# Kernel tuning notes

Measured on AMD Instinct MI355X. Metric: run time of the kernel, lower is better.

Reference implementation:

```python
import jax, jax.numpy as jnp
import numpy as np

B, T, CIN = 64, 1024, 1
H1, H2 = 128, 256  # hidden sizes hardcoded in the flax module


def setup_inputs() -> dict:
    key = jax.random.key(0)
    ks = jax.random.split(key, 24)
    n = lambda k, shp: jax.random.normal(k, shp, dtype=jnp.float32) * 0.05
    z = lambda shp: jnp.zeros(shp, jnp.float32)
    return {
        "X": n(ks[0], (B, T, CIN)),
        "conv_w": n(ks[1], (4, CIN, 16)), "conv_b": z((16,)),
        # gate layout: [i, f, g, o] concatenated, as in flax LSTMCell
        "Wi1": n(ks[2], (16, 4 * H1)), "Wh1": n(ks[3], (H1, 4 * H1)), "b1": z((4 * H1,)),
        "Wi2": n(ks[4], (16, 4 * H1)), "Wh2": n(ks[5], (H1, 4 * H1)), "b2": z((4 * H1,)),
        "Wi3": n(ks[6], (2 * H1, 4 * H2)), "Wh3": n(ks[7], (H2, 4 * H2)), "b3": z((4 * H2,)),
        "Wi4": n(ks[8], (2 * H1, 4 * H2)), "Wh4": n(ks[9], (H2, 4 * H2)), "b4": z((4 * H2,)),
        "attW": n(ks[10], (2 * H2, 128)), "attWb": z((128,)),
        "attV": n(ks[11], (128, 1)), "attVb": z((1,)),
        "d1W": n(ks[12], (2 * H2, 128)), "d1b": z((128,)),
        "d2W": n(ks[13], (128, 1)), "d2b": z((1,)),
    }


def _lstm(x, Wi, Wh, b, hidden):
    """Forward-in-time LSTM over x:(B,T,D) -> outputs (B,T,hidden). flax gate order i,f,g,o."""
    Bb = x.shape[0]

    def step(carry, xt):
        c, h = carry
        z = xt @ Wi + h @ Wh + b  # (B, 4H)
        i, f, g, o = jnp.split(z, 4, axis=-1)
        c = jax.nn.sigmoid(f) * c + jax.nn.sigmoid(i) * jnp.tanh(g)
        h = jax.nn.sigmoid(o) * jnp.tanh(c)
        return (c, h), h

    init = (jnp.zeros((Bb, hidden), x.dtype), jnp.zeros((Bb, hidden), x.dtype))
    _, hs = jax.lax.scan(step, init, jnp.swapaxes(x, 0, 1))  # (T,B,H)
    return jnp.swapaxes(hs, 0, 1)


def reference(X, conv_w, conv_b, Wi1, Wh1, b1, Wi2, Wh2, b2, Wi3, Wh3, b3,
              Wi4, Wh4, b4, attW, attWb, attV, attVb, d1W, d1b, d2W, d2b):
    # Conv1d, SAME padding (flax default)
    x = jax.lax.conv_general_dilated(X, conv_w, (1,), 'SAME',
                                     dimension_numbers=('NWC', 'WIO', 'NWC')) + conv_b
    # NOTE: original flips the FEATURE axis (axis=-1), not time — reproduced faithfully
    x1 = _lstm(x, Wi1, Wh1, b1, H1)
    x2 = _lstm(jnp.flip(x, axis=-1), Wi2, Wh2, b2, H1)
    x = jnp.concatenate([x1, x2], axis=-1)  # (B,T,256)
    x3 = _lstm(x, Wi3, Wh3, b3, H2)
    x4 = _lstm(jnp.flip(x, axis=-1), Wi4, Wh4, b4, H2)
    enc = jnp.concatenate([x3, x4], axis=-1)  # (B,T,512)
    # attention pooling over time
    score = jnp.tanh(enc @ attW + attWb) @ attV + attVb  # (B,T,1)
    w = jax.nn.softmax(score, axis=1)
    ctx = jnp.sum(w * enc, axis=1)  # (B,512)
    h = jnp.tanh(ctx @ d1W + d1b)  # dropout deterministic -> identity
    return h @ d2W + d2b  # (B,1)
```

## Files before the change

### kernel.cpp

```cpp
#include <hip/hip_runtime.h>
#include <hip/hip_fp16.h>

#define B_   64
#define T_   1024
#define H1_  128
#define H2_  256
#define TC_  128
#define NCH  (T_ / TC_)
#define MCH  (B_ * TC_)

typedef unsigned int  u32;
typedef unsigned short u16;
typedef _Float16 half2_t __attribute__((ext_vector_type(2)));

__device__ __forceinline__ float fdot2(u32 w, u32 h, float acc) {
    return __builtin_amdgcn_fdot2(__builtin_bit_cast(half2_t, w),
                                  __builtin_bit_cast(half2_t, h), acc, false);
}
__device__ __forceinline__ u32 pk2(float a, float b) {
    __half2 h = __floats2half2_rn(a, b);
    return __builtin_bit_cast(u32, h);
}
__device__ __forceinline__ float hf(u16 u) { return __half2float(__builtin_bit_cast(__half, u)); }
__device__ __forceinline__ u16 fh(float f) { return __builtin_bit_cast(u16, __float2half(f)); }
__device__ __forceinline__ float sigf(float x) { return 1.0f / (1.0f + expf(-x)); }

__global__ void cvt_all(const float* __restrict__ Wh3, const float* __restrict__ Wh4,
                        const float* __restrict__ Wi3, const float* __restrict__ Wi4,
                        const float* __restrict__ attW,
                        const float* __restrict__ Wh1, const float* __restrict__ Wh2,
                        const float* __restrict__ cw, const float* __restrict__ cb,
                        const float* __restrict__ Wi1, const float* __restrict__ Wi2,
                        const float* __restrict__ b1, const float* __restrict__ b2,
                        u32* __restrict__ wpk, u32* __restrict__ wi3pk,
                        u32* __restrict__ wi4pk, u32* __restrict__ awpk,
                        uint4* __restrict__ wpkT, u32* __restrict__ whs,
                        float* __restrict__ w4s, float* __restrict__ beffs)
{
    int idx = blockIdx.x * 256 + threadIdx.x;
    if (idx < 262144) {
        int l = idx >> 17, rem = idx & 131071, k2 = rem >> 10, j = rem & 1023;
        const float* W = l ? Wh4 : Wh3;
        wpk[idx] = pk2(W[(2 * k2) * 1024 + j], W[(2 * k2 + 1) * 1024 + j]);
    } else if (idx < 393216) {
        int rel = idx - 262144, k2 = rel >> 10, n = rel & 1023;
        wi3pk[rel] = pk2(Wi3[(2 * k2) * 1024 + n], Wi3[(2 * k2 + 1) * 1024 + n]);
    } else if (idx < 524288) {
        int rel = idx - 393216, k2 = rel >> 10, n = rel & 1023;
        wi4pk[rel] = pk2(Wi4[(255 - 2 * k2) * 1024 + n], Wi4[(254 - 2 * k2) * 1024 + n]);
    } else if (idx < 557056) {
        int rel = idx - 524288, k2 = rel >> 7, n = rel & 127;
        awpk[rel] = pk2(attW[(2 * k2) * 128 + n], attW[(2 * k2 + 1) * 128 + n]);
    } else if (idx < 585728) {
        int rel = idx - 557056;
        int l = rel / 14336;
        int rem = rel - l * 14336;
        int q = rem >> 10, col = rem & 1023;
        const float* W = l ? Wh4 : Wh3;
        int k2 = 72 + 4 * q;
        uint4 v;
        v.x = pk2(W[(2 * k2 + 0) * 1024 + col], W[(2 * k2 + 1) * 1024 + col]);
        v.y = pk2(W[(2 * k2 + 2) * 1024 + col], W[(2 * k2 + 3) * 1024 + col]);
        v.z = pk2(W[(2 * k2 + 4) * 1024 + col], W[(2 * k2 + 5) * 1024 + col]);
        v.w = pk2(W[(2 * k2 + 6) * 1024 + col], W[(2 * k2 + 7) * 1024 + col]);
        wpkT[rel] = v;
    } else if (idx < 651264) {
        int rel = idx - 585728;
        int l = rel >> 15, rem = rel & 32767, p = rem >> 9, col = rem & 511;
        const float* W = l ? Wh2 : Wh1;
        whs[rel] = pk2(W[(2 * p) * 512 + col], W[(2 * p + 1) * 512 + col]);
    } else if (idx < 652288) {
        int rel = idx - 651264;
        int l = rel >> 9, col = rel & 511;
        const float* Wi = l ? Wi2 : Wi1;
        const float* bb = l ? b2 : b1;
#pragma unroll
        for (int kk = 0; kk < 4; ++kk) {
            float s = 0.f;
#pragma unroll
            for (int c0 = 0; c0 < 16; ++c0) {
                int cc = l ? (15 - c0) : c0;
                s += cw[kk * 16 + c0] * Wi[cc * 512 + col];
            }
            w4s[(l * 4 + kk) * 512 + col] = s;
        }
        float be = bb[col];
#pragma unroll
        for (int c0 = 0; c0 < 16; ++c0) {
            int cc = l ? (15 - c0) : c0;
            be += cb[c0] * Wi[cc * 512 + col];
        }
        beffs[l * 512 + col] = be;
    }
}

__global__ __launch_bounds__(512) void fused_step(
    const u16* __restrict__ pre, const u32* __restrict__ wpk,
    const uint4* __restrict__ wpkT, float* __restrict__ state,
    u16* __restrict__ enc,
    const float* __restrict__ X, const u32* __restrict__ whs,
    const float* __restrict__ w4s, const float* __restrict__ beffs,
    float* __restrict__ sstC, u16* __restrict__ sstH,
    u16* __restrict__ x12, int c)
{
    __shared__ __align__(16) uint4 wlA[9][512];
    __shared__ __align__(16) uint4 wlB[9][512];
    __shared__ __align__(16) u32 hbuf_pk[128];
    __shared__ float zbuf[1024];
    __shared__ __align__(16) u32 hbs[64];

    const int j = threadIdx.x;

    if (blockIdx.x < 128) {
        if (c == 0) return;
        const int t0 = (c - 1) * TC_;
        const int blk = blockIdx.x;
        const int b = blk >> 1;
        const int layer = blk & 1;

        const u32* wp = wpk + (size_t)layer * 131072;
        u32 wrA[36], wrB[36];
#pragma unroll
        for (int q = 0; q < 36; ++q) {
            wrA[q] = wp[q * 1024 + j];
            wrB[q] = wp[q * 1024 + 512 + j];
        }
#pragma unroll
        for (int m = 0; m < 9; ++m) {
            uint4 va, vb;
            va.x = wp[(36 + 4 * m + 0) * 1024 + j];
            va.y = wp[(36 + 4 * m + 1) * 1024 + j];
            va.z = wp[(36 + 4 * m + 2) * 1024 + j];
            va.w = wp[(36 + 4 * m + 3) * 1024 + j];
            vb.x = wp[(36 + 4 * m + 0) * 1024 + 512 + j];
            vb.y = wp[(36 + 4 * m + 1) * 1024 + 512 + j];
            vb.z = wp[(36 + 4 * m + 2) * 1024 + 512 + j];
            vb.w = wp[(36 + 4 * m + 3) * 1024 + 512 + j];
            wlA[m][j] = va;
            wlB[m][j] = vb;
        }
        const uint4* wt = wpkT + (size_t)layer * 14 * 1024;

        float* st = state + ((size_t)layer * B_ + b) * 512;
        u16* hb16 = (u16*)hbuf_pk;
        float c_state = 0.f, h_last = 0.f;
        if (j < 256) {
            float h0 = (t0 == 0) ? 0.f : st[256 + j];
            c_state = (t0 == 0) ? 0.f : st[j];
            hb16[j] = fh(h0);
            h_last = h0;
        }
        __syncthreads();

        const u16* prow = pre + (size_t)(layer * MCH + b * TC_) * 1024;
        u16* encrow = enc + ((size_t)b * T_ + t0) * 512 + layer * 256;
        const uint4* hp4 = (const uint4*)hbuf_pk;

        for (int tt = 0; tt < TC_; ++tt, prow += 1024, encrow += 512) {
            u16 pA = prow[j], pB = prow[512 + j];
            float a0 = 0.f, a1 = 0.f, b0 = 0.f, b1 = 0.f;
#pragma unroll
            for (int m = 0; m < 9; ++m) {
                uint4 hh = hp4[m];
                a0 = fdot2(wrA[4 * m + 0], hh.x, a0);
                a1 = fdot2(wrA[4 * m + 1], hh.y, a1);
                a0 = fdot2(wrA[4 * m + 2], hh.z, a0);
                a1 = fdot2(wrA[4 * m + 3], hh.w, a1);
                b0 = fdot2(wrB[4 * m + 0], hh.x, b0);
                b1 = fdot2(wrB[4 * m + 1], hh.y, b1);
                b0 = fdot2(wrB[4 * m + 2], hh.z, b0);
                b1 = fdot2(wrB[4 * m + 3], hh.w, b1);
            }
#pragma unroll
            for (int m = 0; m < 9; ++m) {
                uint4 hh = hp4[9 + m];
                uint4 wa = wlA[m][j];
                uint4 wb = wlB[m][j];
                a0 = fdot2(wa.x, hh.x, a0); a1 = fdot2(wa.y, hh.y, a1);
                a0 = fdot2(wa.z, hh.z, a0); a1 = fdot2(wa.w, hh.w, a1);
                b0 = fdot2(wb.x, hh.x, b0); b1 = fdot2(wb.y, hh.y, b1);
                b0 = fdot2(wb.z, hh.z, b0); b1 = fdot2(wb.w, hh.w, b1);
            }
#pragma unroll
            for (int q = 0; q < 14; ++q) {
                uint4 hh = hp4[18 + q];
                uint4 wa = wt[q * 1024 + j];
                uint4 wb = wt[q * 1024 + 512 + j];
                a0 = fdot2(wa.x, hh.x, a0); a1 = fdot2(wa.y, hh.y, a1);
                a0 = fdot2(wa.z, hh.z, a0); a1 = fdot2(wa.w, hh.w, a1);
                b0 = fdot2(wb.x, hh.x, b0); b1 = fdot2(wb.y, hh.y, b1);
                b0 = fdot2(wb.z, hh.z, b0); b1 = fdot2(wb.w, hh.w, b1);
            }
            float zA = (a0 + a1) + hf(pA);
            float zB = (b0 + b1) + hf(pB);
            zbuf[j] = sigf(zA);
            zbuf[512 + j] = (j < 256) ? tanhf(zB) : sigf(zB);
            __syncthreads();
            if (j < 256) {
                float gi = zbuf[j], gf = zbuf[256 + j], gg = zbuf[512 + j], go = zbuf[768 + j];
                c_state = gf * c_state + gi * gg;
                float h = go * tanhf(c_state);
                hb16[j] = fh(h);
                encrow[j] = fh(h);
                h_last = h;
            }
            __syncthreads();
        }
        if (j < 256) { st[j] = c_state; st[256 + j] = h_last; }
    } else {
        if (c >= NCH) return;
        const int chain = blockIdx.x - 128;
        const int b = chain >> 1;
        const int layer = chain & 1;

        float W4[4];
#pragma unroll
        for (int kk = 0; kk < 4; ++kk) W4[kk] = w4s[(layer * 4 + kk) * 512 + j];
        float beff = beffs[layer * 512 + j];
        u32 whp[64];
#pragma unroll
        for (int p = 0; p < 64; ++p) whp[p] = whs[(layer * 64 + p) * 512 + j];

        u16* hb16 = (u16*)hbs;
        float c_state = 0.f;
        if (j < 128) {
            if (c == 0) hb16[j] = 0;
            else { c_state = sstC[chain * 128 + j]; hb16[j] = sstH[chain * 128 + j]; }
        }
        const int t0 = c * TC_;
        const float* Xb = X + (size_t)b * T_;
        float xm1 = (t0 == 0) ? 0.f : Xb[t0 - 1];
        float x0 = Xb[t0], xp1 = Xb[t0 + 1], xp2 = Xb[t0 + 2];
        __syncthreads();

        const uint4* hp4 = (const uint4*)hbs;
        u16 hprev = 0;
        for (int t = t0; t < t0 + TC_; ++t) {
            float xnext = (t + 3 < T_) ? Xb[t + 3] : 0.f;

            float za = beff + xm1 * W4[0] + x0 * W4[1] + xp1 * W4[2] + xp2 * W4[3];
            float zb = 0.f, zc = 0.f, zd = 0.f;
#pragma unroll
            for (int m = 0; m < 16; ++m) {
                uint4 hh = hp4[m];
                za = fdot2(whp[4 * m + 0], hh.x, za);
                zb = fdot2(whp[4 * m + 1], hh.y, zb);
                zc = fdot2(whp[4 * m + 2], hh.z, zc);
                zd = fdot2(whp[4 * m + 3], hh.w, zd);
            }
            float z = (za + zb) + (zc + zd);
            zbuf[j] = (j >= 256 && j < 384) ? tanhf(z) : sigf(z);
            __syncthreads();
            if (j < 128) {
                float gi = zbuf[j], gf = zbuf[128 + j], gg = zbuf[256 + j], go = zbuf[384 + j];
                c_state = gf * c_state + gi * gg;
                float h = go * tanhf(c_state);
                hprev = fh(h);
                hb16[j] = hprev;
                x12[((size_t)b * T_ + t) * 256 + layer * 128 + j] = hprev;
            }
            xm1 = x0; x0 = xp1; xp1 = xp2; xp2 = xnext;
            __syncthreads();
        }
        if (j < 128) { sstC[chain * 128 + j] = c_state; sstH[chain * 128 + j] = hprev; }
    }
}

__global__ __launch_bounds__(256) void gemm2(
    const u16* __restrict__ A, const u32* __restrict__ B3, const u32* __restrict__ B4,
    const float* __restrict__ b3, const float* __restrict__ b4,
    u16* __restrict__ pre, int t0)
{
    __shared__ __align__(16) u32 Apk[8][132];
    __shared__ __align__(16) u32 Bld[8][128];
    const int N = 1024, K = 256;
    const int tid = threadIdx.x;
    const int bx = blockIdx.x;
    const int layer = bx >> 6;
    const int m0 = (bx & 63) * 128;
    const int n0 = blockIdx.y * 128;
    const u32* Bpk = layer ? B4 : B3;
    const float* bias = layer ? b4 : b3;
    u16* outp = pre + (size_t)layer * MCH * 1024;

    const int tm = tid >> 4, tn = tid & 15;
    const int ar = tid >> 1, ap = (tid & 1) * 4;
    const int bkp = tid >> 5, bn4 = (tid & 31) * 4;

    int arow = m0 + ar;
    arow = (arow >> 7) * T_ + t0 + (arow & (TC_ - 1));

    float acc[8][8];
#pragma unroll
    for (int r = 0; r < 8; ++r)
#pragma unroll
        for (int c = 0; c < 8; ++c) acc[r][c] = 0.f;

    for (int k0 = 0; k0 < K; k0 += 16) {
        uint4 ua = *(const uint4*)(A + (size_t)arow * K + k0 + ap * 2);
        uint4 ub = *(const uint4*)(Bpk + (size_t)((k0 >> 1) + bkp) * N + n0 + bn4);
        Apk[ap + 0][ar] = ua.x; Apk[ap + 1][ar] = ua.y;
        Apk[ap + 2][ar] = ua.z; Apk[ap + 3][ar] = ua.w;
        *(uint4*)&Bld[bkp][bn4] = ub;
        __syncthreads();
#pragma unroll
        for (int kp = 0; kp < 8; ++kp) {
            u32 a[8], bp[8];
            *(uint4*)(a)      = *(const uint4*)&Apk[kp][tm * 8];
            *(uint4*)(a + 4)  = *(const uint4*)&Apk[kp][tm * 8 + 4];
            *(uint4*)(bp)     = *(const uint4*)&Bld[kp][tn * 8];
            *(uint4*)(bp + 4) = *(const uint4*)&Bld[kp][tn * 8 + 4];
#pragma unroll
            for (int r = 0; r < 8; ++r)
#pragma unroll
                for (int c = 0; c < 8; ++c)
                    acc[r][c] = fdot2(a[r], bp[c], acc[r][c]);
        }
        __syncthreads();
    }

    float bv[8];
#pragma unroll
    for (int c = 0; c < 8; ++c) bv[c] = bias[n0 + tn * 8 + c];
#pragma unroll
    for (int r = 0; r < 8; ++r) {
        u32 pkv[4];
#pragma unroll
        for (int c2 = 0; c2 < 4; ++c2)
            pkv[c2] = pk2(acc[r][2 * c2] + bv[2 * c2], acc[r][2 * c2 + 1] + bv[2 * c2 + 1]);
        uint4 st = make_uint4(pkv[0], pkv[1], pkv[2], pkv[3]);
        *(uint4*)(outp + (size_t)(m0 + tm * 8 + r) * N + n0 + tn * 8) = st;
    }
}

__global__ __launch_bounds__(256) void gemmS1(
    const u16* __restrict__ A, const u32* __restrict__ Bpk,
    const float* __restrict__ bias, float* __restrict__ outp)
{
    __shared__ __align__(16) u32 Apk[8][132];
    __shared__ __align__(16) u32 Bld[8][128];
    const int N = 128, K = 512;
    const int tid = threadIdx.x;
    const int m0 = blockIdx.x * 128;
    const int n0 = 0;
    const int tm = tid >> 4, tn = tid & 15;
    const int ar = tid >> 1, ap = (tid & 1) * 4;
    const int bkp = tid >> 5, bn4 = (tid & 31) * 4;
    const int arow = m0 + ar;

    float acc[8][8];
#pragma unroll
    for (int r = 0; r < 8; ++r)
#pragma unroll
        for (int c = 0; c < 8; ++c) acc[r][c] = 0.f;

    for (int k0 = 0; k0 < K; k0 += 16) {
        uint4 ua = *(const uint4*)(A + (size_t)arow * K + k0 + ap * 2);
        uint4 ub;
        if (bn4 < N) ub = *(const uint4*)(Bpk + (size_t)((k0 >> 1) + bkp) * N + n0 + bn4);
        else ub = make_uint4(0, 0, 0, 0);
        Apk[ap + 0][ar] = ua.x; Apk[ap + 1][ar] = ua.y;
        Apk[ap + 2][ar] = ua.z; Apk[ap + 3][ar] = ua.w;
        if (bn4 < N) *(uint4*)&Bld[bkp][bn4] = ub;
        __syncthreads();
#pragma unroll
        for (int kp = 0; kp < 8; ++kp) {
            u32 a[8], bp[8];
            *(uint4*)(a)      = *(const uint4*)&Apk[kp][tm * 8];
            *(uint4*)(a + 4)  = *(const uint4*)&Apk[kp][tm * 8 + 4];
            int cb = (tn & 7) * 8 + ((tn >> 3) & 1) * 64;
            cb = (tn * 8) & 127;
            *(uint4*)(bp)     = *(const uint4*)&Bld[kp][cb];
            *(uint4*)(bp + 4) = *(const uint4*)&Bld[kp][cb + 4];
#pragma unroll
            for (int r = 0; r < 8; ++r)
#pragma unroll
                for (int c = 0; c < 8; ++c)
                    acc[r][c] = fdot2(a[r], bp[c], acc[r][c]);
        }
        __syncthreads();
    }

    int ncol = (tn * 8) & 127;
    float bv[8];
#pragma unroll
    for (int c = 0; c < 8; ++c) bv[c] = bias[ncol + c];
    if (tn < 16) {
#pragma unroll
        for (int r = 0; r < 8; ++r) {
            float v[8];
#pragma unroll
            for (int c = 0; c < 8; ++c) v[c] = tanhf(acc[r][c] + bv[c]);
            *(float4*)(outp + (size_t)(m0 + tm * 8 + r) * N + ncol)     = *(float4*)v;
            *(float4*)(outp + (size_t)(m0 + tm * 8 + r) * N + ncol + 4) = *(float4*)(v + 4);
        }
    }
}

__global__ __launch_bounds__(256) void attn_head(
    const float* __restrict__ S1, const u16* __restrict__ enc,
    const float* __restrict__ attV, const float* __restrict__ attVb,
    const float* __restrict__ d1W, const float* __restrict__ d1b,
    const float* __restrict__ d2W, const float* __restrict__ d2b,
    float* __restrict__ out)
{
    const int b = blockIdx.x;
    const int tid = threadIdx.x;
    const int lane = tid & 63, w = tid >> 6;

    __shared__ float sb[1024];
    __shared__ float red[32];
    __shared__ __align__(16) float ctx[512];
    __shared__ float h1s[128];

    float av0 = attV[lane], av1 = attV[64 + lane];
    const float* S1b = S1 + (size_t)b * T_ * 128;
    for (int it = 0; it < 256; ++it) {
        int t = it * 4 + w;
        const float* row = S1b + (size_t)t * 128;
        float p = row[lane] * av0 + row[64 + lane] * av1;
#pragma unroll
        for (int off = 32; off > 0; off >>= 1) p += __shfl_down(p, off);
        if (lane == 0) sb[t] = p + attVb[0];
    }
    __syncthreads();

    float mx = -3.0e38f;
#pragma unroll
    for (int q = 0; q < 4; ++q) mx = fmaxf(mx, sb[tid + 256 * q]);
#pragma unroll
    for (int off = 32; off > 0; off >>= 1) mx = fmaxf(mx, __shfl_down(mx, off));
    if (lane == 0) red[w] = mx;
    __syncthreads();
    if (tid == 0) red[8] = fmaxf(fmaxf(red[0], red[1]), fmaxf(red[2], red[3]));
    __syncthreads();
    float bm = red[8];
    float s = 0.f;
#pragma unroll
    for (int q = 0; q < 4; ++q) {
        float e = expf(sb[tid + 256 * q] - bm);
        sb[tid + 256 * q] = e;
        s += e;
    }
#pragma unroll
    for (int off = 32; off > 0; off >>= 1) s += __shfl_down(s, off);
    if (lane == 0) red[16 + w] = s;
    __syncthreads();
    if (tid == 0) red[24] = 1.0f / (red[16] + red[17] + red[18] + red[19]);
    __syncthreads();
    float inv = red[24];
#pragma unroll
    for (int q = 0; q < 4; ++q) sb[tid + 256 * q] *= inv;
    __syncthreads();

    const u16* encb = enc + (size_t)b * T_ * 512;
    float a0 = 0.f, a1 = 0.f;
    for (int t = 0; t < T_; ++t) {
        float wt = sb[t];
        a0 += wt * hf(encb[(size_t)t * 512 + tid]);
        a1 += wt * hf(encb[(size_t)t * 512 + 256 + tid]);
    }
    ctx[tid] = a0;
    ctx[256 + tid] = a1;
    __syncthreads();

    if (tid < 128) {
        float s1 = d1b[tid];
        for (int k = 0; k < 512; ++k) s1 += ctx[k] * d1W[k * 128 + tid];
        h1s[tid] = tanhf(s1);
    }
    __syncthreads();
    if (tid < 128) {
        float p = h1s[tid] * d2W[tid];
#pragma unroll
        for (int off = 32; off > 0; off >>= 1) p += __shfl_down(p, off);
        if ((tid & 63) == 0) red[28 + (tid >> 6)] = p;
    }
    __syncthreads();
    if (tid == 0) out[b] = red[28] + red[29] + d2b[0];
}

extern "C" void kernel_launch(void* const* d_in, const int* in_sizes, int n_in,
                              void* d_out, int out_size, void* d_ws, size_t ws_size,
                              hipStream_t stream)
{
    const float* X    = (const float*)d_in[0];
    const float* cw   = (const float*)d_in[1];
    const float* cb   = (const float*)d_in[2];
    const float* Wi1  = (const float*)d_in[3];
    const float* Wh1  = (const float*)d_in[4];
    const float* b1   = (const float*)d_in[5];
    const float* Wi2  = (const float*)d_in[6];
    const float* Wh2  = (const float*)d_in[7];
    const float* b2   = (const float*)d_in[8];
    const float* Wi3  = (const float*)d_in[9];
    const float* Wh3  = (const float*)d_in[10];
    const float* b3   = (const float*)d_in[11];
    const float* Wi4  = (const float*)d_in[12];
    const float* Wh4  = (const float*)d_in[13];
    const float* b4   = (const float*)d_in[14];
    const float* attW = (const float*)d_in[15];
    const float* attWb= (const float*)d_in[16];
    const float* attV = (const float*)d_in[17];
    const float* attVb= (const float*)d_in[18];
    const float* d1W  = (const float*)d_in[19];
    const float* d1b  = (const float*)d_in[20];
    const float* d2W  = (const float*)d_in[21];
    const float* d2b  = (const float*)d_in[22];
    float* out = (float*)d_out;

    char* w = (char*)d_ws;
    u16*   x12  = (u16*)w;
    u16*   pre  = (u16*)(w + 33554432);
    u16*   enc  = (u16*)(w + 67108864);
    u32*   wpk  = (u32*)(w + 134217728);
    float* state= (float*)(w + 135266304);
    u32*   wi3pk= (u32*)(w + 135528448);
    u32*   wi4pk= (u32*)(w + 136052736);
    u32*   awpk = (u32*)(w + 136577024);
    uint4* wpkT = (uint4*)(w + 136708096);
    u32*   whs  = (u32*)(w + 137166848);
    float* w4s  = (float*)(w + 137428992);
    float* beffs= (float*)(w + 137445376);
    float* sstC = (float*)(w + 137449472);
    u16*   sstH = (u16*)(w + 137515008);
    float* S1   = (float*)(w + 33554432);

    cvt_all<<<2548, 256, 0, stream>>>(Wh3, Wh4, Wi3, Wi4, attW, Wh1, Wh2, cw, cb,
                                      Wi1, Wi2, b1, b2,
                                      wpk, wi3pk, wi4pk, awpk, wpkT, whs, w4s, beffs);

    for (int c = 0; c <= NCH; ++c) {
        fused_step<<<256, 512, 0, stream>>>(pre, wpk, wpkT, state, enc,
                                            X, whs, w4s, beffs, sstC, sstH, x12, c);
        if (c < NCH)
            gemm2<<<dim3(128, 8), 256, 0, stream>>>(x12, wi3pk, wi4pk, b3, b4, pre, c * TC_);
    }

    gemmS1<<<512, 256, 0, stream>>>(enc, awpk, attWb, S1);
    attn_head<<<64, 256, 0, stream>>>(S1, enc, attV, attVb, d1W, d1b, d2W, d2b, out);
}
```

Baseline: 2.546 ms.

## Replace fdot2 GEMMs with MFMA-based templated GEMM and transpose weight packing

The input-projection GEMM for the layer-3/4 LSTMs and the attention score GEMM move from scalar fdot2 accumulation to the 16x16x32 f16 MFMA matrix instruction in one templated kernel. The Wi3, Wi4 and attW packing switches to an N-major, K-contiguous layout so each lane can load its B fragment directly from shared memory. The goal is to cut the ALU cost of these GEMMs, which run between the sequential recurrence chunks. The trade-off is that output stores become scattered 2-byte and 4-byte writes instead of vectorized rows.

```diff
diff --git a/kernel.cpp b/kernel.cpp
--- a/kernel.cpp
+++ b/kernel.cpp
@@ -12,6 +12,8 @@
 typedef unsigned int  u32;
 typedef unsigned short u16;
 typedef _Float16 half2_t __attribute__((ext_vector_type(2)));
+typedef _Float16 half8 __attribute__((ext_vector_type(8)));
+typedef float f32x4 __attribute__((ext_vector_type(4)));
 
 __device__ __forceinline__ float fdot2(u32 w, u32 h, float acc) {
     return __builtin_amdgcn_fdot2(__builtin_bit_cast(half2_t, w),
@@ -32,8 +34,8 @@
                         const float* __restrict__ cw, const float* __restrict__ cb,
                         const float* __restrict__ Wi1, const float* __restrict__ Wi2,
                         const float* __restrict__ b1, const float* __restrict__ b2,
-                        u32* __restrict__ wpk, u32* __restrict__ wi3pk,
-                        u32* __restrict__ wi4pk, u32* __restrict__ awpk,
+                        u32* __restrict__ wpk, u32* __restrict__ wi3T,
+                        u32* __restrict__ wi4T, u32* __restrict__ awT,
                         uint4* __restrict__ wpkT, u32* __restrict__ whs,
                         float* __restrict__ w4s, float* __restrict__ beffs)
 {
@@ -43,14 +45,14 @@
         const float* W = l ? Wh4 : Wh3;
         wpk[idx] = pk2(W[(2 * k2) * 1024 + j], W[(2 * k2 + 1) * 1024 + j]);
     } else if (idx < 393216) {
-        int rel = idx - 262144, k2 = rel >> 10, n = rel & 1023;
-        wi3pk[rel] = pk2(Wi3[(2 * k2) * 1024 + n], Wi3[(2 * k2 + 1) * 1024 + n]);
+        int rel = idx - 262144, n = rel >> 7, kp = rel & 127;
+        wi3T[rel] = pk2(Wi3[(2 * kp) * 1024 + n], Wi3[(2 * kp + 1) * 1024 + n]);
     } else if (idx < 524288) {
-        int rel = idx - 393216, k2 = rel >> 10, n = rel & 1023;
-        wi4pk[rel] = pk2(Wi4[(255 - 2 * k2) * 1024 + n], Wi4[(254 - 2 * k2) * 1024 + n]);
+        int rel = idx - 393216, n = rel >> 7, kp = rel & 127;
+        wi4T[rel] = pk2(Wi4[(255 - 2 * kp) * 1024 + n], Wi4[(254 - 2 * kp) * 1024 + n]);
     } else if (idx < 557056) {
-        int rel = idx - 524288, k2 = rel >> 7, n = rel & 127;
-        awpk[rel] = pk2(attW[(2 * k2) * 128 + n], attW[(2 * k2 + 1) * 128 + n]);
+        int rel = idx - 524288, n = rel >> 8, kp = rel & 255;
+        awT[rel] = pk2(attW[(2 * kp) * 128 + n], attW[(2 * kp + 1) * 128 + n]);
     } else if (idx < 585728) {
         int rel = idx - 557056;
         int l = rel / 14336;
@@ -266,133 +268,98 @@
     }
 }
 
-__global__ __launch_bounds__(256) void gemm2(
-    const u16* __restrict__ A, const u32* __restrict__ B3, const u32* __restrict__ B4,
-    const float* __restrict__ b3, const float* __restrict__ b4,
-    u16* __restrict__ pre, int t0)
+template<int OUTMODE, int CHUNK, int LAYERED>
+__global__ __launch_bounds__(256) void gemm_mfma(
+    const u16* __restrict__ A, const u32* __restrict__ B0, const u32* __restrict__ B1,
+    const float* __restrict__ bias0, const float* __restrict__ bias1,
+    void* __restrict__ outv, int t0, int N, int K)
 {
-    __shared__ __align__(16) u32 Apk[8][132];
-    __shared__ __align__(16) u32 Bld[8][128];
-    const int N = 1024, K = 256;
+    __shared__ __align__(16) u32 Al[128][20];
+    __shared__ __align__(16) u32 Bl[128][20];
     const int tid = threadIdx.x;
     const int bx = blockIdx.x;
-    const int layer = bx >> 6;
-    const int m0 = (bx & 63) * 128;
+    const int layer = LAYERED ? (bx >> 6) : 0;
+    const int m0 = LAYERED ? ((bx & 63) * 128) : (bx * 128);
     const int n0 = blockIdx.y * 128;
-    const u32* Bpk = layer ? B4 : B3;
-    const float* bias = layer ? b4 : b3;
-    u16* outp = pre + (size_t)layer * MCH * 1024;
-
-    const int tm = tid >> 4, tn = tid & 15;
-    const int ar = tid >> 1, ap = (tid & 1) * 4;
-    const int bkp = tid >> 5, bn4 = (tid & 31) * 4;
-
-    int arow = m0 + ar;
-    arow = (arow >> 7) * T_ + t0 + (arow & (TC_ - 1));
-
-    float acc[8][8];
-#pragma unroll
-    for (int r = 0; r < 8; ++r)
-#pragma unroll
-        for (int c = 0; c < 8; ++c) acc[r][c] = 0.f;
-
-    for (int k0 = 0; k0 < K; k0 += 16) {
-        uint4 ua = *(const uint4*)(A + (size_t)arow * K + k0 + ap * 2);
-        uint4 ub = *(const uint4*)(Bpk + (size_t)((k0 >> 1) + bkp) * N + n0 + bn4);
-        Apk[ap + 0][ar] = ua.x; Apk[ap + 1][ar] = ua.y;
-        Apk[ap + 2][ar] = ua.z; Apk[ap + 3][ar] = ua.w;
-        *(uint4*)&Bld[bkp][bn4] = ub;
+    const u32* Bpk = layer ? B1 : B0;
+    const float* bias = layer ? bias1 : bias0;
+    const int K2 = K >> 1;
+
+    const int w = tid >> 6;
+    const int lane = tid & 63;
+    const int wr = (w >> 1) * 64, wc = (w & 1) * 64;
+    const int lr = lane & 15, lg = lane >> 4;
+
+    f32x4 acc[4][4];
+#pragma unroll
+    for (int r = 0; r < 4; ++r)
+#pragma unroll
+        for (int c = 0; c < 4; ++c) acc[r][c] = (f32x4){0.f, 0.f, 0.f, 0.f};
+
+    for (int k0 = 0; k0 < K; k0 += 32) {
+        const int kp0 = k0 >> 1;
+#pragma unroll
+        for (int it = 0; it < 2; ++it) {
+            int idx = tid + it * 256;
+            int row = idx >> 2, q = idx & 3;
+            int grow = m0 + row;
+            size_t garow = CHUNK ? ((size_t)(grow >> 7) * T_ + t0 + (grow & 127)) : (size_t)grow;
+            uint4 ua = *(const uint4*)(A + garow * K + k0 + q * 8);
+            *(uint4*)&Al[row][q * 4] = ua;
+            uint4 ub = *(const uint4*)(Bpk + (size_t)(n0 + row) * K2 + kp0 + q * 4);
+            *(uint4*)&Bl[row][q * 4] = ub;
+        }
         __syncthreads();
-#pragma unroll
-        for (int kp = 0; kp < 8; ++kp) {
-            u32 a[8], bp[8];
-            *(uint4*)(a)      = *(const uint4*)&Apk[kp][tm * 8];
-            *(uint4*)(a + 4)  = *(const uint4*)&Apk[kp][tm * 8 + 4];
-            *(uint4*)(bp)     = *(const uint4*)&Bld[kp][tn * 8];
-            *(uint4*)(bp + 4) = *(const uint4*)&Bld[kp][tn * 8 + 4];
-#pragma unroll
-            for (int r = 0; r < 8; ++r)
-#pragma unroll
-                for (int c = 0; c < 8; ++c)
-                    acc[r][c] = fdot2(a[r], bp[c], acc[r][c]);
+        half8 bfr[4];
+#pragma unroll
+        for (int c = 0; c < 4; ++c) {
+            const u32* bp = &Bl[wc + c * 16 + lr][0];
+            uint2 blo = *(const uint2*)(bp + 2 * lg);
+            uint2 bhi = *(const uint2*)(bp + 8 + 2 * lg);
+            uint4 bf = make_uint4(blo.x, blo.y, bhi.x, bhi.y);
+            bfr[c] = __builtin_bit_cast(half8, bf);
+        }
+#pragma unroll
+        for (int r = 0; r < 4; ++r) {
+            const u32* ap = &Al[wr + r * 16 + lr][0];
+            uint2 alo = *(const uint2*)(ap + 2 * lg);
+            uint2 ahi = *(const uint2*)(ap + 8 + 2 * lg);
+            uint4 af = make_uint4(alo.x, alo.y, ahi.x, ahi.y);
+            half8 av = __builtin_bit_cast(half8, af);
+#pragma unroll
+            for (int c = 0; c < 4; ++c)
+                acc[r][c] = __builtin_amdgcn_mfma_f32_16x16x32_f16(av, bfr[c], acc[r][c], 0, 0, 0);
         }
         __syncthreads();
     }
 
-    float bv[8];
-#pragma unroll
-    for (int c = 0; c < 8; ++c) bv[c] = bias[n0 + tn * 8 + c];
-#pragma unroll
-    for (int r = 0; r < 8; ++r) {
-        u32 pkv[4];
-#pragma unroll
-        for (int c2 = 0; c2 < 4; ++c2)
-            pkv[c2] = pk2(acc[r][2 * c2] + bv[2 * c2], acc[r][2 * c2 + 1] + bv[2 * c2 + 1]);
-        uint4 st = make_uint4(pkv[0], pkv[1], pkv[2], pkv[3]);
-        *(uint4*)(outp + (size_t)(m0 + tm * 8 + r) * N + n0 + tn * 8) = st;
-    }
-}
-
-__global__ __launch_bounds__(256) void gemmS1(
-    const u16* __restrict__ A, const u32* __restrict__ Bpk,
-    const float* __restrict__ bias, float* __restrict__ outp)
-{
-    __shared__ __align__(16) u32 Apk[8][132];
-    __shared__ __align__(16) u32 Bld[8][128];
-    const int N = 128, K = 512;
-    const int tid = threadIdx.x;
-    const int m0 = blockIdx.x * 128;
-    const int n0 = 0;
-    const int tm = tid >> 4, tn = tid & 15;
-    const int ar = tid >> 1, ap = (tid & 1) * 4;
-    const int bkp = tid >> 5, bn4 = (tid & 31) * 4;
-    const int arow = m0 + ar;
-
-    float acc[8][8];
-#pragma unroll
-    for (int r = 0; r < 8; ++r)
-#pragma unroll
-        for (int c = 0; c < 8; ++c) acc[r][c] = 0.f;
-
-    for (int k0 = 0; k0 < K; k0 += 16) {
-        uint4 ua = *(const uint4*)(A + (size_t)arow * K + k0 + ap * 2);
-        uint4 ub;
-        if (bn4 < N) ub = *(const uint4*)(Bpk + (size_t)((k0 >> 1) + bkp) * N + n0 + bn4);
-        else ub = make_uint4(0, 0, 0, 0);
-        Apk[ap + 0][ar] = ua.x; Apk[ap + 1][ar] = ua.y;
-        Apk[ap + 2][ar] = ua.z; Apk[ap + 3][ar] = ua.w;
-        if (bn4 < N) *(uint4*)&Bld[bkp][bn4] = ub;
-        __syncthreads();
-#pragma unroll
-        for (int kp = 0; kp < 8; ++kp) {
-            u32 a[8], bp[8];
-            *(uint4*)(a)      = *(const uint4*)&Apk[kp][tm * 8];
-            *(uint4*)(a + 4)  = *(const uint4*)&Apk[kp][tm * 8 + 4];
-            int cb = (tn & 7) * 8 + ((tn >> 3) & 1) * 64;
-            cb = (tn * 8) & 127;
-            *(uint4*)(bp)     = *(const uint4*)&Bld[kp][cb];
-            *(uint4*)(bp + 4) = *(const uint4*)&Bld[kp][cb + 4];
-#pragma unroll
-            for (int r = 0; r < 8; ++r)
-#pragma unroll
-                for (int c = 0; c < 8; ++c)
-                    acc[r][c] = fdot2(a[r], bp[c], acc[r][c]);
-        }
-        __syncthreads();
-    }
-
-    int ncol = (tn * 8) & 127;
-    float bv[8];
-#pragma unroll
-    for (int c = 0; c < 8; ++c) bv[c] = bias[ncol + c];
-    if (tn < 16) {
-#pragma unroll
-        for (int r = 0; r < 8; ++r) {
-            float v[8];
-#pragma unroll
-            for (int c = 0; c < 8; ++c) v[c] = tanhf(acc[r][c] + bv[c]);
-            *(float4*)(outp + (size_t)(m0 + tm * 8 + r) * N + ncol)     = *(float4*)v;
-            *(float4*)(outp + (size_t)(m0 + tm * 8 + r) * N + ncol + 4) = *(float4*)(v + 4);
+    if (OUTMODE == 0) {
+        u16* outp = (u16*)outv + (LAYERED ? (size_t)layer * MCH * 1024 : 0);
+#pragma unroll
+        for (int c = 0; c < 4; ++c) {
+            int col = n0 + wc + c * 16 + lr;
+            float bvs = bias[col];
+#pragma unroll
+            for (int r = 0; r < 4; ++r) {
+                int orow = m0 + wr + r * 16 + 4 * lg;
+#pragma unroll
+                for (int i = 0; i < 4; ++i)
+                    outp[(size_t)(orow + i) * N + col] = fh(acc[r][c][i] + bvs);
+            }
+        }
+    } else {
+        float* outp = (float*)outv;
+#pragma unroll
+        for (int c = 0; c < 4; ++c) {
+            int col = n0 + wc + c * 16 + lr;
+            float bvs = bias[col];
+#pragma unroll
+            for (int r = 0; r < 4; ++r) {
+                int orow = m0 + wr + r * 16 + 4 * lg;
+#pragma unroll
+                for (int i = 0; i < 4; ++i)
+                    outp[(size_t)(orow + i) * N + col] = tanhf(acc[r][c][i] + bvs);
+            }
         }
     }
 }
@@ -515,9 +482,9 @@
     u16*   enc  = (u16*)(w + 67108864);
     u32*   wpk  = (u32*)(w + 134217728);
     float* state= (float*)(w + 135266304);
-    u32*   wi3pk= (u32*)(w + 135528448);
-    u32*   wi4pk= (u32*)(w + 136052736);
-    u32*   awpk = (u32*)(w + 136577024);
+    u32*   wi3T = (u32*)(w + 135528448);
+    u32*   wi4T = (u32*)(w + 136052736);
+    u32*   awT  = (u32*)(w + 136577024);
     uint4* wpkT = (uint4*)(w + 136708096);
     u32*   whs  = (u32*)(w + 137166848);
     float* w4s  = (float*)(w + 137428992);
@@ -528,15 +495,17 @@
 
     cvt_all<<<2548, 256, 0, stream>>>(Wh3, Wh4, Wi3, Wi4, attW, Wh1, Wh2, cw, cb,
                                       Wi1, Wi2, b1, b2,
-                                      wpk, wi3pk, wi4pk, awpk, wpkT, whs, w4s, beffs);
+                                      wpk, wi3T, wi4T, awT, wpkT, whs, w4s, beffs);
 
     for (int c = 0; c <= NCH; ++c) {
         fused_step<<<256, 512, 0, stream>>>(pre, wpk, wpkT, state, enc,
                                             X, whs, w4s, beffs, sstC, sstH, x12, c);
         if (c < NCH)
-            gemm2<<<dim3(128, 8), 256, 0, stream>>>(x12, wi3pk, wi4pk, b3, b4, pre, c * TC_);
-    }
-
-    gemmS1<<<512, 256, 0, stream>>>(enc, awpk, attWb, S1);
+            gemm_mfma<0, 1, 1><<<dim3(128, 8), 256, 0, stream>>>(
+                x12, wi3T, wi4T, b3, b4, pre, c * TC_, 1024, 256);
+    }
+
+    gemm_mfma<1, 0, 0><<<dim3(512, 1), 256, 0, stream>>>(
+        enc, awT, awT, attWb, attWb, S1, 0, 128, 512);
     attn_head<<<64, 256, 0, stream>>>(S1, enc, attV, attVb, d1W, d1b, d2W, d2b, out);
 }
```

New measurement: 2.110 ms, median of 2. -17.1%, faster.
